# Performance work log

Hardware: AMD Instinct MI355X
Metric: run time of the kernel (lower is better)

## Reference

```python
import jax, jax.numpy as jnp
import numpy as np
from jax import lax

GEN_POLY = ("1111001", "1011011")  # rate 1/2, constraint length 7 (octal 171/133)


def build_trellis(gen_poly):
    """Feed-forward (non-recursive) convolutional trellis tables.

    State = shift-register contents, most-recent bit is the MSB of the state
    index. Returns int32 tables, each [ns, ni]:
      to_nodes[s, b]        : next state from state s with input bit b
      op_by_fromnode[s, b]  : emitted output-symbol index for (s, b)
      from_nodes[j, m]      : m-th predecessor state of state j
      ip_by_tonode[j, m]    : input bit taken on that predecessor transition
    """
    mu = len(gen_poly[0]) - 1
    ns, ni = 2 ** mu, 2
    g = np.array([[int(c) for c in p] for p in gen_poly])  # [conv_n, mu+1]
    to_nodes = np.zeros((ns, ni), np.int32)
    op_by_fromnode = np.zeros((ns, ni), np.int32)
    from_nodes = np.zeros((ns, ni), np.int32)
    ip_by_tonode = np.zeros((ns, ni), np.int32)
    fill = np.zeros(ns, np.int32)
    for s in range(ns):
        rbits = [(s >> (mu - 1 - j)) & 1 for j in range(mu)]
        for b in range(ni):
            w = np.array([b] + rbits)                 # full window [b, r0..r_{mu-1}]
            obits = (g @ w) % 2                        # output bits, MSB first
            o = int("".join(str(int(x)) for x in obits), 2)
            j = int("".join(str(x) for x in ([b] + rbits[:-1])), 2)
            to_nodes[s, b] = j
            op_by_fromnode[s, b] = o
            from_nodes[j, fill[j]] = s
            ip_by_tonode[j, fill[j]] = b
            fill[j] += 1
    return to_nodes, op_by_fromnode, from_nodes, ip_by_tonode


TO_NODES, OP_BY_FROM, FROM_NODES, IP_BY_TO = build_trellis(GEN_POLY)
CONV_N = len(GEN_POLY)
MU = len(GEN_POLY[0]) - 1
NS = 2 ** MU
NO = 2 ** CONV_N
# output-symbol bit patterns, MSB first, mapped to signs (1-2*bit)
_OP_BITS = np.array([[(o >> (CONV_N - 1 - j)) & 1 for j in range(CONV_N)]
                     for o in range(NO)], np.float32)
OP_SIGN = jnp.asarray(1.0 - 2.0 * _OP_BITS)  # [NO, CONV_N]
IP_SIGN = jnp.asarray([1.0, -1.0])           # sign of input bit b: 1-2b


def setup_inputs() -> dict:
    key = jax.random.key(0)
    k1, k2 = jax.random.split(key)
    B, n = 256, 4096
    T = n // CONV_N  # = k = 2048 info bits
    llr_ch = jax.random.normal(k1, (B, n), dtype=jnp.float32)
    llr_a = jax.random.normal(k2, (B, T), dtype=jnp.float32)
    return {"llr_ch": llr_ch, "llr_a": llr_a}


def _bcjr(llr_ch, llr_a):
    B, n = llr_ch.shape
    T = n // CONV_N
    # branch metrics: bm[t, b, o] = exp(0.5 * sum_j llr[b, t, j] * (1-2*opbit_j(o)))
    llr_r = llr_ch.reshape(B, T, CONV_N)
    bm = jnp.exp(0.5 * jnp.einsum('btj,oj->tbo', llr_r, OP_SIGN))  # [T, B, NO]
    llr_a_t = llr_a.T  # [T, B]

    def gamma_fn(bm_t, la_t):
        # a-priori factor exp(0.5*llr_a*(1-2b)) times channel branch metric
        ap = jnp.exp(0.5 * la_t[:, None, None] * IP_SIGN[None, None, :])  # [B,1,2]
        return ap * bm_t[:, OP_BY_FROM]  # [B, NS, 2]

    alpha0 = jnp.zeros((B, NS), jnp.float32).at[:, 0].set(1.0)

    def fwd(alpha_prev, inp):
        bm_t, la_t = inp
        gam = gamma_fn(bm_t, la_t)                        # [B, NS, 2] by from-state
        ag = gam * alpha_prev[:, :, None]                  # alpha_{t} * gamma_t
        agt = ag[:, FROM_NODES, IP_BY_TO]                  # regroup by to-state
        alpha = agt.sum(-1)
        alpha = alpha / alpha.sum(-1, keepdims=True)       # normalize (as in TF code)
        return alpha, alpha_prev                            # emit alpha BEFORE step t

    _, alphas = lax.scan(fwd, alpha0, (bm, llr_a_t))       # alphas[t] = alpha_t, [T,B,NS]

    beta_T = jnp.full((B, NS), 1.0 / NS, jnp.float32)      # non-terminated: uniform

    def bwd(beta_next, inp):
        bm_t, la_t, alpha_t = inp
        gam = gamma_fn(bm_t, la_t)                         # [B, NS, 2]
        bg = gam * beta_next[:, TO_NODES]                  # gamma * beta_{t+1}(to)
        beta = bg.sum(-1)
        beta = beta / beta.sum(-1, keepdims=True)
        joint = alpha_t[:, :, None] * bg                   # APP per (state, bit)
        llr_t = jnp.log(joint[..., 0].sum(-1)) - jnp.log(joint[..., 1].sum(-1))
        return beta, llr_t

    _, llrs_rev = lax.scan(bwd, beta_T, (bm[::-1], llr_a_t[::-1], alphas[::-1]))
    return llrs_rev[::-1].T  # [B, T] soft LLRs (hard_out=False)


def reference(llr_ch, llr_a):
    return _bcjr(llr_ch, llr_a)
```

## Files before the change

kernel.cpp:

```cpp
#include <hip/hip_runtime.h>

#define T_LEN 2048
#define NSTATE 64
#define NCHUNK 16
#define CH_S 128
#define WARM 64
#define RK 16

template<int CTRL>
__device__ __forceinline__ float dpp_add(float v) {
    int r = __builtin_amdgcn_update_dpp(0, __float_as_int(v), CTRL, 0xF, 0xF, true);
    return v + __int_as_float(r);
}

__device__ __forceinline__ float wave_sum64(float v) {
    v = dpp_add<0xB1>(v);
    v = dpp_add<0x4E>(v);
    v = dpp_add<0x124>(v);
    v = dpp_add<0x128>(v);
    v += __shfl_xor(v, 16, 64);
    v += __shfl_xor(v, 32, 64);
    return v;
}

__device__ __forceinline__ float pair_sum_xor1(float v) {
    int r = __builtin_amdgcn_update_dpp(0, __float_as_int(v), 0xB1, 0xF, 0xF, true);
    return v + __int_as_float(r);
}

__device__ __forceinline__ unsigned short bf16_of(float f) {
    return (unsigned short)((__float_as_uint(f) + 0x8000u) >> 16);
}


__global__ __launch_bounds__(256, 4)
void bcjr_fwd_kernel(const float* __restrict__ llr_ch,
                     const float* __restrict__ llr_a,
                     unsigned short* __restrict__ wsA)
{
    const int wave  = blockIdx.x * 4 + (threadIdx.x >> 6);
    const int lane  = threadIdx.x & 63;
    const int chunk = wave & (NCHUNK - 1);
    const int b     = wave >> 4;

    const float c0 = 1.0f - 2.0f * (float)(__popc(lane & 57) & 1);
    const float c1 = 1.0f - 2.0f * (float)(__popc(lane & 27) & 1);
    const float kE = 0.5f * 1.442695040888963f;
    const float k0 = kE * c0, k1 = kE * c1;

    const float* chp = llr_ch + (size_t)b * (2 * T_LEN);
    const float* lap = llr_a  + (size_t)b * T_LEN;
    unsigned short* w = wsA + (size_t)b * T_LEN * NSTATE;

    const int  fs0 = 2 * (lane & 31);
    const bool fhi = (lane >= 32);
    const int t0 = chunk * CH_S;
    const int ts = (chunk == 0) ? t0 : t0 - WARM;
    float state = (chunk == 0) ? ((lane == 0) ? 1.0f : 0.0f) : (1.0f / 64.0f);

    for (int g = ts; g < t0 + CH_S; g += RK) {
        const bool store = (g >= t0);
        #pragma unroll
        for (int h = 0; h < 2; ++h) {
            const int gb = g + 8 * h;
            const float4* c4 = (const float4*)(chp + 2 * gb);
            const float4* a4 = (const float4*)(lap + gb);
            float4 cc[4], aa[2];
            #pragma unroll
            for (int i = 0; i < 4; ++i) cc[i] = c4[i];
            #pragma unroll
            for (int i = 0; i < 2; ++i) aa[i] = a4[i];
            unsigned short* wb = w + (size_t)gb * NSTATE + lane;
            #pragma unroll
            for (int i = 0; i < 8; ++i) {
                float l0 = (i & 1) ? cc[i >> 1].z : cc[i >> 1].x;
                float l1 = (i & 1) ? cc[i >> 1].w : cc[i >> 1].y;
                float la = ((const float*)aa)[i];
                if (store) wb[i * NSTATE] = bf16_of(state);
                float x   = fmaf(la, kE, fmaf(l0, k0, l1 * k1));
                float g0v = exp2f(x);
                float g1v = __builtin_amdgcn_rcpf(g0v);
                float s0  = pair_sum_xor1(state * g0v);
                float s1  = pair_sum_xor1(state * g1v);
                float a0  = __shfl(s0, fs0, 64);
                float a1  = __shfl(s1, fs0, 64);
                state = fhi ? a1 : a0;
            }
        }
        float s = wave_sum64(state);
        state = state * __builtin_amdgcn_rcpf(s);
    }
}

__global__ __launch_bounds__(256, 4)
void bcjr_bwd_llr_kernel(const float* __restrict__ llr_ch,
                         const float* __restrict__ llr_a,
                         const unsigned short* __restrict__ wsA,
                         float* __restrict__ out)
{
    const int wave  = blockIdx.x * 4 + (threadIdx.x >> 6);
    const int lane  = threadIdx.x & 63;
    const int chunk = wave & (NCHUNK - 1);
    const int b     = wave >> 4;

    const float c0 = 1.0f - 2.0f * (float)(__popc(lane & 57) & 1);
    const float c1 = 1.0f - 2.0f * (float)(__popc(lane & 27) & 1);
    const float kE = 0.5f * 1.442695040888963f;
    const float k0 = kE * c0, k1 = kE * c1;

    const float* chp = llr_ch + (size_t)b * (2 * T_LEN);
    const float* lap = llr_a  + (size_t)b * T_LEN;
    const unsigned short* wa = wsA + (size_t)b * T_LEN * NSTATE;
    float* outp = out + (size_t)b * T_LEN;

    const int  bs0 = lane >> 1;
    const int  bs1 = 32 + (lane >> 1);
    const bool fhi = (lane >= 32);
    const int t0 = chunk * CH_S;
    const int te = (chunk == NCHUNK - 1) ? (t0 + CH_S) : (t0 + CH_S + WARM);
    float state = 1.0f / 64.0f;

    for (int g = te - RK; g >= t0; g -= RK) {
        const bool act = (g < t0 + CH_S);
        #pragma unroll
        for (int h = 1; h >= 0; --h) {
            const int gb = g + 8 * h;
            const float4* c4 = (const float4*)(chp + 2 * gb);
            const float4* a4 = (const float4*)(lap + gb);
            float4 cc[4], aa[2];
            #pragma unroll
            for (int i = 0; i < 4; ++i) cc[i] = c4[i];
            #pragma unroll
            for (int i = 0; i < 2; ++i) aa[i] = a4[i];
            float av[8];
            if (act) {
                const unsigned short* ap = wa + (size_t)gb * NSTATE + lane;
                #pragma unroll
                for (int i = 0; i < 8; ++i)
                    av[i] = __uint_as_float(((unsigned)ap[i * NSTATE]) << 16);
            }
            #pragma unroll
            for (int i = 7; i >= 0; --i) {
                float l0 = (i & 1) ? cc[i >> 1].z : cc[i >> 1].x;
                float l1 = (i & 1) ? cc[i >> 1].w : cc[i >> 1].y;
                float la = ((const float*)aa)[i];
                float x   = fmaf(la, kE, fmaf(l0, k0, l1 * k1));
                float g0v = exp2f(x);
                float g1v = __builtin_amdgcn_rcpf(g0v);
                float t0v = __shfl(state, bs0, 64);
                float t1v = __shfl(state, bs1, 64);
                float p0 = g0v * t0v;
                float p1 = g1v * t1v;
                if (act) {
                    float na = av[i] * p0;
                    float nb = av[i] * p1;
                    na += __shfl_xor(na, 32, 64);
                    nb += __shfl_xor(nb, 32, 64);
                    float z = fhi ? nb : na;
                    z = dpp_add<0xB1>(z);
                    z = dpp_add<0x4E>(z);
                    z = dpp_add<0x124>(z);
                    z = dpp_add<0x128>(z);
                    z += __shfl_xor(z, 16, 64);
                    float lg = __log2f(z);
                    float d  = (lg - __shfl_xor(lg, 32, 64)) * 0.6931471805599453f;
                    if (lane == 0) outp[gb + i] = d;
                }
                state = p0 + p1;
            }
        }
        float s = wave_sum64(state);
        state = state * __builtin_amdgcn_rcpf(s);
    }
}

extern "C" void kernel_launch(void* const* d_in, const int* in_sizes, int n_in,
                              void* d_out, int out_size, void* d_ws, size_t ws_size,
                              hipStream_t stream) {
    const float* llr_ch = (const float*)d_in[0];
    const float* llr_a  = (const float*)d_in[1];
    float* out = (float*)d_out;

    int B = in_sizes[0] / (2 * T_LEN);
    unsigned short* wsA = (unsigned short*)d_ws;

    int n_waves = B * NCHUNK;
    hipLaunchKernelGGL(bcjr_fwd_kernel, dim3(n_waves / 4), dim3(256), 0, stream,
                       llr_ch, llr_a, wsA);
    hipLaunchKernelGGL(bcjr_bwd_llr_kernel, dim3(n_waves / 4), dim3(256), 0, stream,
                       llr_ch, llr_a, wsA, out);
}
```

Measured before the change: 147.5 us.

## Halve chunk length, double waves, and use DPP row-broadcast reductions

Splits each sequence into 32 chunks of 64 steps instead of 16 chunks of 128, doubling the number of waves to expose more parallelism, and raises the occupancy hint in launch bounds. Wave reductions now use a DPP row_shr/row_bcast prefix sum ending in lane 63 followed by readlane, replacing the shuffle-xor steps. The backward LLR computation does two independent DPP reductions with no cross-half shuffles and writes from lane 63. Shorter chunks keep the 64-step warmup, so the share of redundant warmup work rises.

```diff
diff --git a/kernel.cpp b/kernel.cpp
--- a/kernel.cpp
+++ b/kernel.cpp
@@ -2,8 +2,8 @@
 
 #define T_LEN 2048
 #define NSTATE 64
-#define NCHUNK 16
-#define CH_S 128
+#define NCHUNK 32
+#define CH_S 64
 #define WARM 64
 #define RK 16
 
@@ -13,14 +13,19 @@
     return v + __int_as_float(r);
 }
 
-__device__ __forceinline__ float wave_sum64(float v) {
-    v = dpp_add<0xB1>(v);
-    v = dpp_add<0x4E>(v);
-    v = dpp_add<0x124>(v);
-    v = dpp_add<0x128>(v);
-    v += __shfl_xor(v, 16, 64);
-    v += __shfl_xor(v, 32, 64);
+__device__ __forceinline__ float dpp_sum_to63(float v) {
+    v = dpp_add<0x111>(v);
+    v = dpp_add<0x112>(v);
+    v = dpp_add<0x114>(v);
+    v = dpp_add<0x118>(v);
+    v = dpp_add<0x142>(v);
+    v = dpp_add<0x143>(v);
     return v;
+}
+
+__device__ __forceinline__ float wave_total(float v) {
+    float s = dpp_sum_to63(v);
+    return __int_as_float(__builtin_amdgcn_readlane(__float_as_int(s), 63));
 }
 
 __device__ __forceinline__ float pair_sum_xor1(float v) {
@@ -33,7 +38,7 @@
 }
 
 
-__global__ __launch_bounds__(256, 4)
+__global__ __launch_bounds__(256, 8)
 void bcjr_fwd_kernel(const float* __restrict__ llr_ch,
                      const float* __restrict__ llr_a,
                      unsigned short* __restrict__ wsA)
@@ -41,7 +46,7 @@
     const int wave  = blockIdx.x * 4 + (threadIdx.x >> 6);
     const int lane  = threadIdx.x & 63;
     const int chunk = wave & (NCHUNK - 1);
-    const int b     = wave >> 4;
+    const int b     = wave >> 5;
 
     const float c0 = 1.0f - 2.0f * (float)(__popc(lane & 57) & 1);
     const float c1 = 1.0f - 2.0f * (float)(__popc(lane & 27) & 1);
@@ -87,12 +92,12 @@
                 state = fhi ? a1 : a0;
             }
         }
-        float s = wave_sum64(state);
+        float s = wave_total(state);
         state = state * __builtin_amdgcn_rcpf(s);
     }
 }
 
-__global__ __launch_bounds__(256, 4)
+__global__ __launch_bounds__(256, 8)
 void bcjr_bwd_llr_kernel(const float* __restrict__ llr_ch,
                          const float* __restrict__ llr_a,
                          const unsigned short* __restrict__ wsA,
@@ -101,7 +106,7 @@
     const int wave  = blockIdx.x * 4 + (threadIdx.x >> 6);
     const int lane  = threadIdx.x & 63;
     const int chunk = wave & (NCHUNK - 1);
-    const int b     = wave >> 4;
+    const int b     = wave >> 5;
 
     const float c0 = 1.0f - 2.0f * (float)(__popc(lane & 57) & 1);
     const float c1 = 1.0f - 2.0f * (float)(__popc(lane & 27) & 1);
@@ -115,7 +120,6 @@
 
     const int  bs0 = lane >> 1;
     const int  bs1 = 32 + (lane >> 1);
-    const bool fhi = (lane >= 32);
     const int t0 = chunk * CH_S;
     const int te = (chunk == NCHUNK - 1) ? (t0 + CH_S) : (t0 + CH_S + WARM);
     float state = 1.0f / 64.0f;
@@ -152,24 +156,15 @@
                 float p0 = g0v * t0v;
                 float p1 = g1v * t1v;
                 if (act) {
-                    float na = av[i] * p0;
-                    float nb = av[i] * p1;
-                    na += __shfl_xor(na, 32, 64);
-                    nb += __shfl_xor(nb, 32, 64);
-                    float z = fhi ? nb : na;
-                    z = dpp_add<0xB1>(z);
-                    z = dpp_add<0x4E>(z);
-                    z = dpp_add<0x124>(z);
-                    z = dpp_add<0x128>(z);
-                    z += __shfl_xor(z, 16, 64);
-                    float lg = __log2f(z);
-                    float d  = (lg - __shfl_xor(lg, 32, 64)) * 0.6931471805599453f;
-                    if (lane == 0) outp[gb + i] = d;
+                    float na = dpp_sum_to63(av[i] * p0);
+                    float nb = dpp_sum_to63(av[i] * p1);
+                    float d  = (__log2f(na) - __log2f(nb)) * 0.6931471805599453f;
+                    if (lane == 63) outp[gb + i] = d;
                 }
                 state = p0 + p1;
             }
         }
-        float s = wave_sum64(state);
+        float s = wave_total(state);
         state = state * __builtin_amdgcn_rcpf(s);
     }
 }
```

New measurement: 151.0 us. 1.02x slower.
